# Kernel optimization log

Measured on AMD Instinct MI355X. Metric: run time of the kernel, lower is better.

## Reference

```python
import jax, jax.numpy as jnp
import numpy as np

N_TARGETS = 21
R_HW = 7
FM_H, FM_W = 64, 64
N_ROIS = 300


def setup_inputs() -> dict:
    key = jax.random.key(0)
    k1, k2, k3, k4 = jax.random.split(key, 4)
    FM = jax.random.normal(k1, (N_TARGETS * R_HW ** 2, FM_H, FM_W), dtype=jnp.float32)
    # Build valid ROIs (x1, y1, x2, y2) in feature-map pixel coordinates.
    x1 = jax.random.uniform(k2, (N_ROIS,), minval=0.0, maxval=FM_W * 0.6)
    y1 = jax.random.uniform(k3, (N_ROIS,), minval=0.0, maxval=FM_H * 0.6)
    wh = jax.random.uniform(k4, (N_ROIS, 2), minval=R_HW, maxval=FM_W * 0.4)
    x2 = jnp.minimum(x1 + wh[:, 0], FM_W - 1.0)
    y2 = jnp.minimum(y1 + wh[:, 1], FM_H - 1.0)
    rois = jnp.stack([x1, y1, x2, y2], axis=1).astype(jnp.float32)
    return {"FM": FM, "rois": rois, "n_targets": N_TARGETS, "r_hw": R_HW}


def _bin_masks(start, length, r_hw, size, dtype):
    """start, length: [R]; returns [R, r_hw, size] float bin-membership masks."""
    p = jnp.arange(r_hw, dtype=dtype)
    bin_sz = length / r_hw  # [R]
    lo = jnp.floor(start[:, None] + p[None, :] * bin_sz[:, None])          # [R, r_hw]
    hi = jnp.ceil(start[:, None] + (p[None, :] + 1.0) * bin_sz[:, None])   # [R, r_hw]
    lo = jnp.clip(lo, 0.0, size)
    hi = jnp.clip(hi, 0.0, size)
    idx = jnp.arange(size, dtype=dtype)
    mask = (idx[None, None, :] >= lo[:, :, None]) & (idx[None, None, :] < hi[:, :, None])
    return mask.astype(dtype)


def reference(FM, rois, n_targets, r_hw):
    """Position-sensitive ROI pooling (R-FCN).
    FM: [n_targets*r_hw^2, H, W]; rois: [R, 4] as (x1, y1, x2, y2).
    Returns pooled: [R, n_targets, r_hw, r_hw].
    Bin (p, q) of target t averages FM channel t*r_hw^2 + p*r_hw + q over the
    pixels in that bin; empty bins yield 0.
    """
    C, H, W = FM.shape
    dtype = FM.dtype
    FMr = FM.reshape(n_targets, r_hw, r_hw, H, W)  # [t, p, q, h, w]
    x1, y1, x2, y2 = rois[:, 0], rois[:, 1], rois[:, 2], rois[:, 3]
    roi_h = jnp.maximum(y2 - y1, 0.1)
    roi_w = jnp.maximum(x2 - x1, 0.1)
    mask_h = _bin_masks(y1, roi_h, r_hw, H, dtype)  # [R, p, H]
    mask_w = _bin_masks(x1, roi_w, r_hw, W, dtype)  # [R, q, W]
    # Sum over w per output column q, then over h per output row p.
    tmp = jnp.einsum('tpqhw,rqw->rtpqh', FMr, mask_w)
    s = jnp.einsum('rtpqh,rph->rtpq', tmp, mask_h)
    cnt = mask_h.sum(-1)[:, None, :, None] * mask_w.sum(-1)[:, None, None, :]  # [R,1,p,q]
    return s / jnp.maximum(cnt, 1.0)
```

## Files before the change

kernel.cpp:

```cpp
#include <hip/hip_runtime.h>


#define N_TARGETS 21
#define R_HW 7
#define FM_H 64
#define FM_W 64
#define PLANE (FM_H * FM_W)
#define CPT (N_TARGETS * R_HW * R_HW)

typedef __attribute__((address_space(3))) float lds_f32;
typedef __attribute__((address_space(1))) const float glb_f32;

struct Geo {
  int w0, w1, h0, h1, a;
  float inv;
};

__device__ __forceinline__ Geo roi_geom(const float4 rv, int p, int q) {
  Geo g;
  const float x1 = rv.x, y1 = rv.y, x2 = rv.z, y2 = rv.w;
  const float bw = fmaxf(x2 - x1, 0.1f) / (float)R_HW;
  const float bh = fmaxf(y2 - y1, 0.1f) / (float)R_HW;

  const float lo_wf = fminf(fmaxf(floorf(x1 + (float)q * bw), 0.0f), (float)FM_W);
  const float hi_wf = fminf(fmaxf(ceilf (x1 + ((float)q + 1.0f) * bw), 0.0f), (float)FM_W);
  const float lo_hf = fminf(fmaxf(floorf(y1 + (float)p * bh), 0.0f), (float)FM_H);
  const float hi_hf = fminf(fmaxf(ceilf (y1 + ((float)p + 1.0f) * bh), 0.0f), (float)FM_H);

  g.w0 = (int)lo_wf; g.w1 = (int)hi_wf;
  g.h0 = (int)lo_hf; g.h1 = (int)hi_hf;
  const int cnt = max(g.h1 - g.h0, 0) * max(g.w1 - g.w0, 0);
  g.a = min(g.w0 & ~3, FM_W - 4);
  g.inv = 1.0f / (float)(cnt > 0 ? cnt : 1);
  return g;
}

__device__ __forceinline__ float window_sum(const float* __restrict__ sm,
                                            const Geo g) {
  const int a2 = min(g.a + 4, FM_W - 4);
  float s = 0.0f;
#pragma unroll
  for (int i = 0; i < 5; ++i) {
    const int h  = g.h0 + i;
    const int hc = min(h, FM_H - 1);
    const bool hin = (h < g.h1);
    const float* __restrict__ row = &sm[hc << 6];
    const float4 v0 = *reinterpret_cast<const float4*>(row + g.a);
    const float4 v1 = *reinterpret_cast<const float4*>(row + a2);

    float rs = 0.0f;
    int w;
    w = g.a + 0;  rs += (w >= g.w0 && w < g.w1) ? v0.x : 0.0f;
    w = g.a + 1;  rs += (w >= g.w0 && w < g.w1) ? v0.y : 0.0f;
    w = g.a + 2;  rs += (w >= g.w0 && w < g.w1) ? v0.z : 0.0f;
    w = g.a + 3;  rs += (w >= g.w0 && w < g.w1) ? v0.w : 0.0f;
    w = g.a + 4;  rs += (w >= g.w0 && w < g.w1) ? v1.x : 0.0f;
    w = g.a + 5;  rs += (w >= g.w0 && w < g.w1) ? v1.y : 0.0f;
    w = g.a + 6;  rs += (w >= g.w0 && w < g.w1) ? v1.z : 0.0f;
    w = g.a + 7;  rs += (w >= g.w0 && w < g.w1) ? v1.w : 0.0f;

    s += hin ? rs : 0.0f;
  }
  return s;
}

__global__ __launch_bounds__(256) void psroi_kernel(
    const float* __restrict__ FM,
    const float* __restrict__ rois,
    float* __restrict__ tmp,
    int n_rois) {
  __shared__ float sm[PLANE];

  const int c   = blockIdx.x;
  const int tid = threadIdx.x;

  const float* __restrict__ plane = FM + (size_t)c * PLANE;
#pragma unroll
  for (int i = 0; i < 4; ++i) {
    const int off = (i * 256 + tid) * 4;
    __builtin_amdgcn_global_load_lds((glb_f32*)(plane + off),
                                     (lds_f32*)(&sm[off]),
                                     16, 0, 0);
  }

  const int pq = c % (R_HW * R_HW);
  const int p  = pq / R_HW;
  const int q  = pq % R_HW;

  const int r0 = tid;
  const int r1 = tid + 256;
  const bool has0 = (r0 < n_rois);
  const bool has1 = (r1 < n_rois);

  Geo g0, g1;
  if (has0) g0 = roi_geom(reinterpret_cast<const float4*>(rois)[r0], p, q);
  if (has1) g1 = roi_geom(reinterpret_cast<const float4*>(rois)[r1], p, q);

  __syncthreads();

  float* __restrict__ trow = tmp + (size_t)c * n_rois;
  if (has0) {
    const float s = window_sum(sm, g0);
    trow[r0] = s * g0.inv;
  }
  if (has1) {
    const float s = window_sum(sm, g1);
    trow[r1] = s * g1.inv;
  }
}

__global__ __launch_bounds__(256) void transpose_kernel(
    const float* __restrict__ tmp,
    float* __restrict__ out,
    int n_rois) {
  __shared__ float tile[32][33];
  const int tx = threadIdx.x;
  const int ty = threadIdx.y;
  const int c0 = blockIdx.x * 32;
  const int rr0 = blockIdx.y * 32;

#pragma unroll
  for (int i = 0; i < 4; ++i) {
    const int c = c0 + ty + i * 8;
    const int r = rr0 + tx;
    if (c < CPT && r < n_rois)
      tile[ty + i * 8][tx] = tmp[(size_t)c * n_rois + r];
  }
  __syncthreads();
#pragma unroll
  for (int i = 0; i < 4; ++i) {
    const int r = rr0 + ty + i * 8;
    const int c = c0 + tx;
    if (r < n_rois && c < CPT)
      out[(size_t)r * CPT + c] = tile[tx][ty + i * 8];
  }
}

extern "C" void kernel_launch(void* const* d_in, const int* in_sizes, int n_in,
                              void* d_out, int out_size, void* d_ws, size_t ws_size,
                              hipStream_t stream) {
  const float* FM   = (const float*)d_in[0];
  const float* rois = (const float*)d_in[1];
  float* out = (float*)d_out;
  float* tmp = (float*)d_ws;

  int n_rois = in_sizes[1] / 4;

  psroi_kernel<<<CPT, 256, 0, stream>>>(FM, rois, tmp, n_rois);

  dim3 tgrid((CPT + 31) / 32, (n_rois + 31) / 32);
  transpose_kernel<<<tgrid, dim3(32, 8), 0, stream>>>(tmp, out, n_rois);
}
```

Before: 72.19 us.

## Fuse transpose into pooling kernel and process two channels per block

Drops the separate transpose kernel and the workspace round-trip by writing pooled values directly into the [R, C] output layout. Each block now handles two adjacent channels, loading the second plane into LDS while the first is being summed. The exchange is strided 8-byte scattered writes to the output instead of coalesced ones, half as many blocks, and doubled LDS per block.

```diff
diff --git a/kernel.cpp b/kernel.cpp
--- a/kernel.cpp
+++ b/kernel.cpp
@@ -67,72 +67,76 @@
 __global__ __launch_bounds__(256) void psroi_kernel(
     const float* __restrict__ FM,
     const float* __restrict__ rois,
-    float* __restrict__ tmp,
+    float* __restrict__ out,
     int n_rois) {
-  __shared__ float sm[PLANE];
+  __shared__ float sm[2][PLANE];
 
-  const int c   = blockIdx.x;
   const int tid = threadIdx.x;
+  const int c0  = blockIdx.x * 2;
+  const int c1  = c0 + 1;
+  const bool have1 = (c1 < CPT);
 
-  const float* __restrict__ plane = FM + (size_t)c * PLANE;
+  const float* __restrict__ plane0 = FM + (size_t)c0 * PLANE;
 #pragma unroll
   for (int i = 0; i < 4; ++i) {
     const int off = (i * 256 + tid) * 4;
-    __builtin_amdgcn_global_load_lds((glb_f32*)(plane + off),
-                                     (lds_f32*)(&sm[off]),
+    __builtin_amdgcn_global_load_lds((glb_f32*)(plane0 + off),
+                                     (lds_f32*)(&sm[0][off]),
                                      16, 0, 0);
   }
 
-  const int pq = c % (R_HW * R_HW);
-  const int p  = pq / R_HW;
-  const int q  = pq % R_HW;
+  const int pq0 = c0 % (R_HW * R_HW);
+  const int p0  = pq0 / R_HW, q0 = pq0 % R_HW;
+  const int pq1 = c1 % (R_HW * R_HW);
+  const int p1  = pq1 / R_HW, q1 = pq1 % R_HW;
 
   const int r0 = tid;
   const int r1 = tid + 256;
-  const bool has0 = (r0 < n_rois);
-  const bool has1 = (r1 < n_rois);
+  const bool hasR0 = (r0 < n_rois);
+  const bool hasR1 = (r1 < n_rois);
 
-  Geo g0, g1;
-  if (has0) g0 = roi_geom(reinterpret_cast<const float4*>(rois)[r0], p, q);
-  if (has1) g1 = roi_geom(reinterpret_cast<const float4*>(rois)[r1], p, q);
+  Geo g00, g01, g10, g11;
+  if (hasR0) {
+    const float4 rv = reinterpret_cast<const float4*>(rois)[r0];
+    g00 = roi_geom(rv, p0, q0);
+    g10 = roi_geom(rv, p1, q1);
+  }
+  if (hasR1) {
+    const float4 rv = reinterpret_cast<const float4*>(rois)[r1];
+    g01 = roi_geom(rv, p0, q0);
+    g11 = roi_geom(rv, p1, q1);
+  }
 
   __syncthreads();
 
-  float* __restrict__ trow = tmp + (size_t)c * n_rois;
-  if (has0) {
-    const float s = window_sum(sm, g0);
-    trow[r0] = s * g0.inv;
+  if (have1) {
+    const float* __restrict__ plane1 = FM + (size_t)c1 * PLANE;
+#pragma unroll
+    for (int i = 0; i < 4; ++i) {
+      const int off = (i * 256 + tid) * 4;
+      __builtin_amdgcn_global_load_lds((glb_f32*)(plane1 + off),
+                                       (lds_f32*)(&sm[1][off]),
+                                       16, 0, 0);
+    }
   }
-  if (has1) {
-    const float s = window_sum(sm, g1);
-    trow[r1] = s * g1.inv;
+
+  float s00 = 0.0f, s01 = 0.0f;
+  if (hasR0) s00 = window_sum(sm[0], g00) * g00.inv;
+  if (hasR1) s01 = window_sum(sm[0], g01) * g01.inv;
+
+  __syncthreads();
+
+  float s10 = 0.0f, s11 = 0.0f;
+  if (have1) {
+    if (hasR0) s10 = window_sum(sm[1], g10) * g10.inv;
+    if (hasR1) s11 = window_sum(sm[1], g11) * g11.inv;
   }
-}
 
-__global__ __launch_bounds__(256) void transpose_kernel(
-    const float* __restrict__ tmp,
-    float* __restrict__ out,
-    int n_rois) {
-  __shared__ float tile[32][33];
-  const int tx = threadIdx.x;
-  const int ty = threadIdx.y;
-  const int c0 = blockIdx.x * 32;
-  const int rr0 = blockIdx.y * 32;
-
-#pragma unroll
-  for (int i = 0; i < 4; ++i) {
-    const int c = c0 + ty + i * 8;
-    const int r = rr0 + tx;
-    if (c < CPT && r < n_rois)
-      tile[ty + i * 8][tx] = tmp[(size_t)c * n_rois + r];
-  }
-  __syncthreads();
-#pragma unroll
-  for (int i = 0; i < 4; ++i) {
-    const int r = rr0 + ty + i * 8;
-    const int c = c0 + tx;
-    if (r < n_rois && c < CPT)
-      out[(size_t)r * CPT + c] = tile[tx][ty + i * 8];
+  if (hasR0) out[(size_t)r0 * CPT + c0] = s00;
+  if (hasR1) out[(size_t)r1 * CPT + c0] = s01;
+  if (have1) {
+    if (hasR0) out[(size_t)r0 * CPT + c1] = s10;
+    if (hasR1) out[(size_t)r1 * CPT + c1] = s11;
   }
 }
 
@@ -142,12 +146,9 @@
   const float* FM   = (const float*)d_in[0];
   const float* rois = (const float*)d_in[1];
   float* out = (float*)d_out;
-  float* tmp = (float*)d_ws;
 
   int n_rois = in_sizes[1] / 4;
 
-  psroi_kernel<<<CPT, 256, 0, stream>>>(FM, rois, tmp, n_rois);
-
-  dim3 tgrid((CPT + 31) / 32, (n_rois + 31) / 32);
-  transpose_kernel<<<tgrid, dim3(32, 8), 0, stream>>>(tmp, out, n_rois);
+  const int nblocks = (CPT + 1) / 2;
+  psroi_kernel<<<nblocks, 256, 0, stream>>>(FM, rois, out, n_rois);
 }
```

Result: no change. 71.81 us (-0.5%).
